# Performance work log

Measured on AMD Instinct MI355X. Metric: run time of the kernel, lower is better.

## Reference

```python
import jax, jax.numpy as jnp
import numpy as np


def _gru_dir(x, Wih, Whh, bih, bhh):
    # x: (B,T,I) -> (B,T,H); torch GRU equations, h0 = 0
    H = Whh.shape[1]
    pre = x @ Wih.T + bih  # (B,T,3H), input projection hoisted out of scan
    def step(h, p):
        gh = h @ Whh.T + bhh
        pr, pz, pn = jnp.split(p, 3, axis=-1)
        gr, gz, gn = jnp.split(gh, 3, axis=-1)
        r = jax.nn.sigmoid(pr + gr)
        z = jax.nn.sigmoid(pz + gz)
        n = jnp.tanh(pn + r * gn)
        h = (1.0 - z) * n + z * h
        return h, h
    h0 = jnp.zeros((x.shape[0], H), x.dtype)
    _, ys = jax.lax.scan(step, h0, jnp.swapaxes(pre, 0, 1))
    return jnp.swapaxes(ys, 0, 1)


def _gru_bidir(x, Wih, Whh, bih, bhh):
    f = _gru_dir(x, Wih[0], Whh[0], bih[0], bhh[0])
    b = _gru_dir(x[:, ::-1], Wih[1], Whh[1], bih[1], bhh[1])[:, ::-1]
    return jnp.concatenate([f, b], axis=-1)


def _forward(inputs, embed, l_Wih, l_Whh, l_bih, l_bhh, r_Wih, r_Whh, r_bih, r_bhh,
             a_Wih, a_Whh, a_bih, a_bhh, Wc1, Wc2, vc, Wb, Wd, vd, Wm, vm, Ws, vs,
             Wp, vp, Wpred):
    x = embed[inputs]  # (B,T,E)
    hl = _gru_bidir(x, l_Wih, l_Whh, l_bih, l_bhh)  # (B,T,2H)
    hr = _gru_bidir(x, r_Wih, r_Whh, r_bih, r_bhh)  # (B,T,2H)
    # co-attention: score[b,i,j] = vc . tanh(Wc1 hl_j + Wc2 hr_i)
    s = jnp.tanh((hl @ Wc1.T)[:, None, :, :] + (hr @ Wc2.T)[:, :, None, :])  # (B,T,T,H)
    ptc = jax.nn.softmax((s @ vc.T)[..., 0], axis=-1) @ hl
    # bilinear: hr (Wb hl)^T
    sjt = jnp.einsum('bid,bjd->bij', hr, hl @ Wb.T)
    ptb = jax.nn.softmax(sjt, axis=-1) @ hl
    # multiplicative: vd . tanh(Wd (hl_j * hr_i))
    p = hl[:, None, :, :] * hr[:, :, None, :]  # (B,T,T,2H)
    ptd = jax.nn.softmax((jnp.tanh(p @ Wd.T) @ vd.T)[..., 0], axis=-1) @ hl
    # subtractive: vm . tanh(Wm (hl_j - hr_i))
    d = hl[:, None, :, :] - hr[:, :, None, :]  # (B,T,T,2H)
    ptm = jax.nn.softmax((jnp.tanh(d @ Wm.T) @ vm.T)[..., 0], axis=-1) @ hl
    # self-attention on hr: vs . tanh(Ws (hr_j * hr_i))
    ss = hr[:, None, :, :] * hr[:, :, None, :]  # (B,T,T,2H)
    pts = jax.nn.softmax((jnp.tanh(ss @ Ws.T) @ vs.T)[..., 0], axis=-1) @ hr
    agg = jnp.concatenate([hr, pts, ptc, ptd, ptb, ptm], axis=-1)  # (B,T,12H)
    ar = _gru_bidir(agg, a_Wih, a_Whh, a_bih, a_bhh)  # (B,T,2H)
    # pooling of hl
    sj = jax.nn.softmax(jnp.swapaxes(jnp.tanh(hl @ Wp.T) @ vp.T, 1, 2), axis=-1)  # (B,1,T)
    rl = sj @ hl  # (B,1,2H)
    # final attention over aggregation
    sj2 = jax.nn.softmax(jnp.swapaxes((ar @ Wc1.T + rl @ Wc2.T) @ vc.T, 1, 2), axis=-1)  # (B,1,T)
    rr = (sj2 @ ar)[:, 0, :]  # (B,2H)
    return jax.nn.sigmoid(rr @ Wpred.T)  # (B,labels)


def setup_inputs() -> dict:
    B, T, V, E, H, L = 4, 256, 30000, 300, 128, 2
    key = jax.random.key(0)
    ks = jax.random.split(key, 40)
    inp = {}
    inp['inputs'] = jax.random.randint(ks[0], (B, T), 0, V)
    inp['embed'] = jax.random.uniform(ks[1], (V, E), jnp.float32, -0.1, 0.1)
    ki = 2
    for name, isz in [('l', E), ('r', E), ('a', 12 * H)]:
        inp[name + '_Wih'] = jax.random.normal(ks[ki], (2, 3 * H, isz), jnp.float32) * 0.05; ki += 1
        inp[name + '_Whh'] = jax.random.normal(ks[ki], (2, 3 * H, H), jnp.float32) * 0.05; ki += 1
        inp[name + '_bih'] = jnp.zeros((2, 3 * H), jnp.float32)
        inp[name + '_bhh'] = jnp.zeros((2, 3 * H), jnp.float32)
    for n, o, i in [('Wc1', H, 2 * H), ('Wc2', H, 2 * H), ('vc', 1, H), ('Wb', 2 * H, 2 * H),
                    ('Wd', H, 2 * H), ('vd', 1, H), ('Wm', H, 2 * H), ('vm', 1, H),
                    ('Ws', H, 2 * H), ('vs', 1, H), ('Wp', H, 2 * H), ('vp', 1, H),
                    ('Wpred', L, 2 * H)]:
        inp[n] = jax.random.normal(ks[ki], (o, i), jnp.float32) * 0.05; ki += 1
    return inp


def reference(inputs, embed, l_Wih, l_Whh, l_bih, l_bhh, r_Wih, r_Whh, r_bih, r_bhh,
              a_Wih, a_Whh, a_bih, a_bhh, Wc1, Wc2, vc, Wb, Wd, vd, Wm, vm, Ws, vs,
              Wp, vp, Wpred):
    return _forward(inputs, embed, l_Wih, l_Whh, l_bih, l_bhh, r_Wih, r_Whh, r_bih,
                    r_bhh, a_Wih, a_Whh, a_bih, a_bhh, Wc1, Wc2, vc, Wb, Wd, vd, Wm,
                    vm, Ws, vs, Wp, vp, Wpred)
```

## Files before the change

kernel.cpp:

```cpp
#include <hip/hip_runtime.h>


#define DEV static __device__ __forceinline__
#define BAR_LGKM() __asm__ volatile("s_waitcnt lgkmcnt(0)\ns_barrier" ::: "memory")

typedef __attribute__((ext_vector_type(4))) float f32x4;
typedef __attribute__((ext_vector_type(8))) short s16x8;
typedef __attribute__((ext_vector_type(4))) unsigned int u32x4;

constexpr int T = 256, E = 300, EP = 320, H = 128, H2 = 256, H3 = 384, H12 = 1536;
constexpr int M = 1024;
constexpr int STY = 262144;

DEV float b2f(unsigned short h) { return __uint_as_float(((unsigned)h) << 16); }
DEV unsigned short f2b(float f) {
  unsigned u = __float_as_uint(f);
  u += 0x7fff + ((u >> 16) & 1);
  return (unsigned short)(u >> 16);
}
DEV unsigned cvt_pk_bf16(float lo, float hi) {
  unsigned r;
  __asm__("v_cvt_pk_bf16_f32 %0, %1, %2" : "=v"(r) : "v"(lo), "v"(hi));
  return r;
}
DEV float rcp_f(float x) {
  float r;
  __asm__("v_rcp_f32 %0, %1" : "=v"(r) : "v"(x));
  return r;
}
DEV float sigm(float x) { return rcp_f(1.f + __expf(-x)); }
DEV float tanh_f(float x) {
  float e = __expf(2.f * x);
  return __builtin_fmaf(-2.f, rcp_f(e + 1.f), 1.f);
}

DEV s16x8 ldfrag(const unsigned short* p) {
  u32x4 v = *(const u32x4*)p;
  return __builtin_bit_cast(s16x8, v);
}
DEV f32x4 mfma16(s16x8 a, s16x8 b, f32x4 c) {
  return __builtin_amdgcn_mfma_f32_16x16x32_bf16(a, b, c, 0, 0, 0);
}


struct StageArgs {
  const float* cs[9]; unsigned short* cd[9]; int cn[9];
  const int* idx; const float* emb; unsigned short* xhi; unsigned short* xlo;
  const float* lW; const float* rW; unsigned short* wpad;
};

__global__ void k_stage(StageArgs sa) {
  int seg = blockIdx.y;
  int i = blockIdx.x * 256 + threadIdx.x;
  if (seg < 9) {
    if (i < sa.cn[seg]) sa.cd[seg][i] = f2b(sa.cs[seg][i]);
    return;
  }
  if (seg == 9) {
    if (i >= M * EP) return;
    int m = i / EP, e = i - m * EP;
    int r = sa.idx[m];
    float v = (e < E) ? sa.emb[(size_t)r * E + e] : 0.f;
    unsigned short hi = f2b(v);
    sa.xhi[i] = hi;
    sa.xlo[i] = f2b(v - b2f(hi));
    return;
  }
  if (i >= 4 * H3 * EP) return;
  int e = i % EP, n = (i / EP) % H3, uu = i / (EP * H3);
  const float* src = (uu < 2 ? sa.lW : sa.rW) + (size_t)((uu & 1) * H3 + n) * E;
  sa.wpad[i] = (e < E) ? f2b(src[e]) : (unsigned short)0;
}


struct GemmDesc {
  const unsigned short* Ahi; const unsigned short* Alo; const unsigned short* W;
  const float* bias; float* Cf; int N; int K;
};
struct GemmBatch { GemmDesc d[8]; };

__global__ __launch_bounds__(256) void k_gemm(GemmBatch gb) {
  GemmDesc g = gb.d[blockIdx.z];
  int nb = blockIdx.y * 64;
  if (nb >= g.N) return;
  int mb = blockIdx.x * 64;
  int lane = threadIdx.x & 63, w = threadIdx.x >> 6, quad = lane >> 4, l16 = lane & 15;
  int K = g.K;
  const unsigned short* Ahp = g.Ahi + (size_t)(mb + w * 16 + l16) * K + quad * 8;
  const unsigned short* Alp = g.Alo + (size_t)(mb + w * 16 + l16) * K + quad * 8;
  const unsigned short* Wp = g.W + (size_t)(nb + l16) * K + quad * 8;
  f32x4 acc[4];
  #pragma unroll
  for (int nt = 0; nt < 4; ++nt) acc[nt] = f32x4{0.f, 0.f, 0.f, 0.f};
  for (int k = 0; k < K; k += 32) {
    s16x8 ah = ldfrag(Ahp + k);
    s16x8 al = ldfrag(Alp + k);
    #pragma unroll
    for (int nt = 0; nt < 4; ++nt) {
      s16x8 b = ldfrag(Wp + (size_t)nt * 16 * K + k);
      acc[nt] = mfma16(ah, b, acc[nt]);
      acc[nt] = mfma16(al, b, acc[nt]);
    }
  }
  int mr0 = mb + w * 16 + quad * 4;
  #pragma unroll
  for (int nt = 0; nt < 4; ++nt) {
    int col = nb + nt * 16 + l16;
    float bv = g.bias ? g.bias[col] : 0.f;
    #pragma unroll
    for (int r = 0; r < 4; ++r)
      g.Cf[(size_t)(mr0 + r) * g.N + col] = acc[nt][r] + bv;
  }
}


struct RecArgs {
  const unsigned short* whh[4];
  const float* pre[4];
  float* outf[4];
  unsigned short* outhi[4];
  unsigned short* outlo[4];
  unsigned short* agghi[4];
  unsigned short* agglo[4];
  const float* bhh[4];
  int colOff[4];
  int dir[4];
};

__global__ __launch_bounds__(512) void k_gru(RecArgs ra) {
  int u = blockIdx.x;
  __shared__ __align__(16) unsigned short hs[2][16 * 136];
  int tid = threadIdx.x, lane = tid & 63, w8 = tid >> 6;
  int quad = lane >> 4, l16 = lane & 15;
  for (int i = tid; i < 2 * 16 * 136; i += 512) ((unsigned short*)hs)[i] = 0;
  const unsigned short* whh = ra.whh[u];
  s16x8 bq[3][4];
  #pragma unroll
  for (int g = 0; g < 3; ++g) {
    int row = g * 128 + w8 * 16 + l16;
    #pragma unroll
    for (int kc = 0; kc < 4; ++kc)
      bq[g][kc] = ldfrag(whh + (size_t)row * H + kc * 32 + quad * 8);
  }
  const float* bhh = ra.bhh[u];
  const float* pre = ra.pre[u];
  float* outf = ra.outf[u];
  unsigned short* outhi = ra.outhi[u];
  unsigned short* outlo = ra.outlo[u];
  unsigned short* agghi = ra.agghi[u];
  unsigned short* agglo = ra.agglo[u];
  int colOff = ra.colOff[u], dir = ra.dir[u];
  int b = ((quad & 1) << 1) | (quad >> 1);
  int d = w8 * 16 + l16;
  float bh_r = bhh[d], bh_z = bhh[d + 128], bh_n = bhh[d + 256];
  float hf = 0.f;
  float ob[8];
  unsigned short obh[8], obl[8];
  int t0 = dir ? (T - 1) : 0;
  const float* pq = pre + (size_t)(b * T + t0) * H3 + d;
  float n_pr = pq[0], n_pz = pq[128], n_pn = pq[256];
  long pst = dir ? -(long)H3 : (long)H3;
  __syncthreads();
  for (int sb = 0; sb < T; sb += 8) {
    #pragma unroll
    for (int ss = 0; ss < 8; ++ss) {
      float pr = n_pr, pz = n_pz, pn = n_pn;
      pq += pst;
      n_pr = pq[0]; n_pz = pq[128]; n_pn = pq[256];
      const unsigned short* hcur = hs[ss & 1];
      unsigned short* hnxt = hs[(ss & 1) ^ 1];
      s16x8 ah[4];
      #pragma unroll
      for (int kc = 0; kc < 4; ++kc)
        ah[kc] = ldfrag(hcur + l16 * 136 + kc * 32 + quad * 8);
      f32x4 accA[3], accB[3];
      #pragma unroll
      for (int g = 0; g < 3; ++g) {
        accA[g] = f32x4{0.f, 0.f, 0.f, 0.f};
        accB[g] = f32x4{0.f, 0.f, 0.f, 0.f};
      }
      #pragma unroll
      for (int g = 0; g < 3; ++g) accA[g] = mfma16(ah[0], bq[g][0], accA[g]);
      #pragma unroll
      for (int g = 0; g < 3; ++g) accB[g] = mfma16(ah[2], bq[g][2], accB[g]);
      #pragma unroll
      for (int g = 0; g < 3; ++g) accA[g] = mfma16(ah[1], bq[g][1], accA[g]);
      #pragma unroll
      for (int g = 0; g < 3; ++g) accB[g] = mfma16(ah[3], bq[g][3], accB[g]);
      float ghv[3];
      #pragma unroll
      for (int g = 0; g < 3; ++g) {
        float x0 = (accA[g][0] + accB[g][0]) + (accA[g][1] + accB[g][1]);
        float x1 = (accA[g][2] + accB[g][2]) + (accA[g][3] + accB[g][3]);
        float y1 = __shfl_xor(x1, 32);
        ghv[g] = (quad >= 2) ? y1 : x0;
      }
      float rg = sigm(pr + ghv[0] + bh_r);
      float zg = sigm(pz + ghv[1] + bh_z);
      float ng = tanh_f(pn + rg * (ghv[2] + bh_n));
      hf = (1.f - zg) * ng + zg * hf;
      unsigned short hi = f2b(hf);
      unsigned short lo = f2b(hf - b2f(hi));
      hnxt[(2 * b) * 136 + d] = hi;
      hnxt[(2 * b + 1) * 136 + d] = lo;
      ob[ss] = hf; obh[ss] = hi; obl[ss] = lo;
      BAR_LGKM();
    }
    #pragma unroll
    for (int qq = 0; qq < 8; ++qq) {
      int sq = sb + qq;
      int tq = dir ? (T - 1 - sq) : sq;
      size_t o = (size_t)(b * T + tq) * H2 + colOff + d;
      outf[o] = ob[qq]; outhi[o] = obh[qq]; outlo[o] = obl[qq];
      if (agghi) {
        size_t a = (size_t)(b * T + tq) * H12 + colOff + d;
        agghi[a] = obh[qq]; agglo[a] = obl[qq];
      }
    }
  }
}


struct ScArgs {
  const unsigned short* Xhi[2];
  const float* Rf; const float* Wt[2]; const float* vt[2];
  float* So[2]; float* So2[2];
  const float *Hc, *Rc, *Hm, *Rm, *HB, *hrf, *vcf, *vmf; float* S;
};

__global__ __launch_bounds__(256, 4) void k_score(ScArgs a) {
  __shared__ __align__(16) unsigned char smem[34816];
  int which = blockIdx.y;
  int bi = blockIdx.x, b = bi >> 8;
  int tid = threadIdx.x;
  if (which == 4) {
    float* rc_l = (float*)smem;
    float* rm_l = rc_l + 128;
    float* vc_l = rm_l + 128;
    float* vm_l = vc_l + 128;
    float* hr_l = vm_l + 128;
    if (tid < 128) {
      rc_l[tid] = a.Rc[(size_t)bi * 128 + tid];
      rm_l[tid] = a.Rm[(size_t)bi * 128 + tid];
      vc_l[tid] = a.vcf[tid];
      vm_l[tid] = a.vmf[tid];
    }
    hr_l[tid] = a.hrf[(size_t)bi * 256 + tid];
    __syncthreads();
    int j = tid;
    const float4* hc4 = (const float4*)(a.Hc + (size_t)(b * 256 + j) * 128);
    const float4* hm4 = (const float4*)(a.Hm + (size_t)(b * 256 + j) * 128);
    const float4* hb4 = (const float4*)(a.HB + (size_t)(b * 256 + j) * 256);
    const float4* rc4 = (const float4*)rc_l;
    const float4* rm4 = (const float4*)rm_l;
    const float4* vc4 = (const float4*)vc_l;
    const float4* vm4 = (const float4*)vm_l;
    const float4* hr4 = (const float4*)hr_l;
    float sc = 0.f, sm = 0.f, sb2 = 0.f;
    #pragma unroll 4
    for (int k = 0; k < 32; ++k) {
      float4 x = hc4[k], c = rc4[k], v = vc4[k];
      sc += v.x * tanh_f(x.x + c.x) + v.y * tanh_f(x.y + c.y)
          + v.z * tanh_f(x.z + c.z) + v.w * tanh_f(x.w + c.w);
      float4 am = hm4[k], cm = rm4[k], vv = vm4[k];
      sm += vv.x * tanh_f(am.x - cm.x) + vv.y * tanh_f(am.y - cm.y)
          + vv.z * tanh_f(am.z - cm.z) + vv.w * tanh_f(am.w - cm.w);
    }
    #pragma unroll 4
    for (int k = 0; k < 64; ++k) {
      float4 p = hb4[k], h = hr4[k];
      sb2 += p.x * h.x + p.y * h.y + p.z * h.z + p.w * h.w;
    }
    size_t o = (size_t)bi * 256 + j;
    a.S[(size_t)STY * 1 + o] = sc;
    a.S[(size_t)STY * 3 + o] = sb2;
    a.S[(size_t)STY * 4 + o] = sm;
    return;
  }
  int type = which >> 1, khb = which & 1;
  const unsigned short* Xhi = a.Xhi[type];
  const float* W = a.Wt[type] + (size_t)khb * 64 * 256;
  const float* v = a.vt[type] + khb * 64;
  float* Sout = khb ? a.So2[type] : a.So[type];
  unsigned short* w_lds = (unsigned short*)smem;
  float* sp = (float*)(smem + 32768);
  int lane = tid & 63, w = tid >> 6, quad = lane >> 4, l16 = lane & 15;
  int cp = w & 1, jh = w >> 1;
  int d4 = tid & 63, rhi = tid >> 6;
  float4 h4 = ((const float4*)(a.Rf + (size_t)bi * 256))[d4];
  #pragma unroll
  for (int it = 0; it < 16; ++it) {
    int kl = it * 4 + rhi;
    float4 w4 = ((const float4*)(W + (size_t)kl * 256))[d4];
    unsigned lo32 = cvt_pk_bf16(w4.x * h4.x, w4.y * h4.y);
    unsigned hi32 = cvt_pk_bf16(w4.z * h4.z, w4.w * h4.w);
    unsigned long long pk = (unsigned long long)lo32 | ((unsigned long long)hi32 << 32);
    int gphys = ((d4 >> 1) + kl) & 31;
    *(unsigned long long*)(w_lds + (size_t)kl * 256 + gphys * 8 + (d4 & 1) * 4) = pk;
  }
  BAR_LGKM();
  s16x8 afr[2][8];
  #pragma unroll
  for (int c = 0; c < 2; ++c) {
    int krow = cp * 32 + c * 16 + l16;
    #pragma unroll
    for (int kc = 0; kc < 8; ++kc) {
      int gp = (kc * 4 + quad + krow) & 31;
      afr[c][kc] = ldfrag(w_lds + (size_t)krow * 256 + gp * 8);
    }
  }
  float vv[2][4];
  #pragma unroll
  for (int c = 0; c < 2; ++c)
    #pragma unroll
    for (int r = 0; r < 4; ++r) vv[c][r] = v[cp * 32 + c * 16 + quad * 4 + r];
  #pragma unroll
  for (int jj = 0; jj < 8; ++jj) {
    int jt = jh * 8 + jj;
    const unsigned short* Xp = Xhi + (size_t)(b * 256 + jt * 16 + l16) * 256 + quad * 8;
    s16x8 bf[8];
    #pragma unroll
    for (int kc = 0; kc < 8; ++kc) bf[kc] = ldfrag(Xp + kc * 32);
    f32x4 acc[2];
    acc[0] = f32x4{0.f, 0.f, 0.f, 0.f};
    acc[1] = f32x4{0.f, 0.f, 0.f, 0.f};
    #pragma unroll
    for (int kc = 0; kc < 8; ++kc) {
      acc[0] = mfma16(afr[0][kc], bf[kc], acc[0]);
      acc[1] = mfma16(afr[1][kc], bf[kc], acc[1]);
    }
    float s = 0.f;
    #pragma unroll
    for (int c = 0; c < 2; ++c)
      #pragma unroll
      for (int r = 0; r < 4; ++r) s += tanh_f(acc[c][r]) * vv[c][r];
    s += __shfl_xor(s, 16);
    s += __shfl_xor(s, 32);
    if (lane < 16) sp[cp * 256 + jt * 16 + l16] = s;
  }
  BAR_LGKM();
  Sout[(size_t)bi * 256 + tid] = sp[tid] + sp[256 + tid];
}


__global__ __launch_bounds__(256) void k_wsum(const float* __restrict__ S,
    const float* __restrict__ S2,
    const float* __restrict__ hl_f, const float* __restrict__ hr_f,
    unsigned short* __restrict__ ahi, unsigned short* __restrict__ alo) {
  int it = blockIdx.x, type = blockIdx.y, b = blockIdx.z;
  __shared__ float p_l[8][256];
  __shared__ float red[4];
  int tid = threadIdx.x;
  for (int ii = 0; ii < 8; ++ii) {
    size_t idx = ((size_t)(b * 256 + it * 8 + ii)) * 256 + tid;
    float x = S[(size_t)type * STY + idx];
    if (type == 0) x += S2[idx];
    else if (type == 2) x += S2[(size_t)STY + idx];
    float m = x;
    for (int dl = 32; dl; dl >>= 1) m = fmaxf(m, __shfl_xor(m, dl));
    if ((tid & 63) == 0) red[tid >> 6] = m;
    __syncthreads();
    m = fmaxf(fmaxf(red[0], red[1]), fmaxf(red[2], red[3]));
    __syncthreads();
    float e = __expf(x - m);
    float sum = e;
    for (int dl = 32; dl; dl >>= 1) sum += __shfl_xor(sum, dl);
    if ((tid & 63) == 0) red[tid >> 6] = sum;
    __syncthreads();
    sum = red[0] + red[1] + red[2] + red[3];
    p_l[ii][tid] = e * rcp_f(sum);
    __syncthreads();
  }
  const float* src = (type == 0 ? hr_f : hl_f) + (size_t)b * 256 * 256;
  float acc[8] = {0.f, 0.f, 0.f, 0.f, 0.f, 0.f, 0.f, 0.f};
  for (int j = 0; j < 256; ++j) {
    float hv = src[(size_t)j * 256 + tid];
    #pragma unroll
    for (int ii = 0; ii < 8; ++ii) acc[ii] += p_l[ii][j] * hv;
  }
  int off = 256 * (1 + type);
  #pragma unroll
  for (int ii = 0; ii < 8; ++ii) {
    float vv = acc[ii];
    unsigned short hi = f2b(vv);
    size_t o = (size_t)(b * 256 + it * 8 + ii) * H12 + off + tid;
    ahi[o] = hi;
    alo[o] = f2b(vv - b2f(hi));
  }
}


__global__ __launch_bounds__(256) void k_tail(const float* __restrict__ Hp,
    const float* __restrict__ hl_f, const float* __restrict__ vpf,
    const float* __restrict__ Wc2f, const float* __restrict__ Arc,
    const float* __restrict__ ar_f, const float* __restrict__ vcf,
    const float* __restrict__ Wpredf, float* __restrict__ out) {
  int b = blockIdx.x, tid = threadIdx.x;
  __shared__ float vl[128], wl[256], rvec[256], rlcl[128], red[4];
  if (tid < 128) vl[tid] = vpf[tid];
  __syncthreads();
  const float* hp = Hp + (size_t)(b * 256 + tid) * 128;
  float s = 0.f;
  for (int k = 0; k < 128; ++k) s += vl[k] * tanh_f(hp[k]);
  float m = s;
  for (int dl = 32; dl; dl >>= 1) m = fmaxf(m, __shfl_xor(m, dl));
  if ((tid & 63) == 0) red[tid >> 6] = m;
  __syncthreads();
  m = fmaxf(fmaxf(red[0], red[1]), fmaxf(red[2], red[3]));
  __syncthreads();
  float e = __expf(s - m);
  float sum = e;
  for (int dl = 32; dl; dl >>= 1) sum += __shfl_xor(sum, dl);
  if ((tid & 63) == 0) red[tid >> 6] = sum;
  __syncthreads();
  sum = red[0] + red[1] + red[2] + red[3];
  wl[tid] = e * rcp_f(sum);
  __syncthreads();
  float acc = 0.f;
  for (int t = 0; t < 256; ++t) acc += wl[t] * hl_f[(size_t)(b * 256 + t) * 256 + tid];
  rvec[tid] = acc;
  __syncthreads();
  if (tid < 128) {
    float a2 = 0.f;
    const float* wr = Wc2f + (size_t)tid * 256;
    for (int dk = 0; dk < 256; ++dk) a2 += rvec[dk] * wr[dk];
    rlcl[tid] = a2;
    vl[tid] = vcf[tid];
  }
  __syncthreads();
  const float* ap = Arc + (size_t)(b * 256 + tid) * 128;
  float s2 = 0.f;
  for (int k = 0; k < 128; ++k) s2 += vl[k] * (ap[k] + rlcl[k]);
  m = s2;
  for (int dl = 32; dl; dl >>= 1) m = fmaxf(m, __shfl_xor(m, dl));
  if ((tid & 63) == 0) red[tid >> 6] = m;
  __syncthreads();
  m = fmaxf(fmaxf(red[0], red[1]), fmaxf(red[2], red[3]));
  __syncthreads();
  float e2 = __expf(s2 - m);
  float sum2 = e2;
  for (int dl = 32; dl; dl >>= 1) sum2 += __shfl_xor(sum2, dl);
  if ((tid & 63) == 0) red[tid >> 6] = sum2;
  __syncthreads();
  sum2 = red[0] + red[1] + red[2] + red[3];
  wl[tid] = e2 * rcp_f(sum2);
  __syncthreads();
  float acc2 = 0.f;
  for (int t = 0; t < 256; ++t) acc2 += wl[t] * ar_f[(size_t)(b * 256 + t) * 256 + tid];
  rvec[tid] = acc2;
  __syncthreads();
  if (tid < 2) {
    float o = 0.f;
    const float* wp = Wpredf + (size_t)tid * 256;
    for (int dk = 0; dk < 256; ++dk) o += rvec[dk] * wp[dk];
    out[b * 2 + tid] = sigm(o);
  }
}


extern "C" void kernel_launch(void* const* d_in, const int* in_sizes, int n_in,
                              void* d_out, int out_size, void* d_ws, size_t ws_size,
                              hipStream_t stream) {
  (void)in_sizes; (void)n_in; (void)out_size; (void)ws_size;
  const int* inputs = (const int*)d_in[0];
  const float* embed = (const float*)d_in[1];
  const float* lWih = (const float*)d_in[2];
  const float* lWhh = (const float*)d_in[3];
  const float* lbih = (const float*)d_in[4];
  const float* lbhh = (const float*)d_in[5];
  const float* rWih = (const float*)d_in[6];
  const float* rWhh = (const float*)d_in[7];
  const float* rbih = (const float*)d_in[8];
  const float* rbhh = (const float*)d_in[9];
  const float* aWih = (const float*)d_in[10];
  const float* aWhh = (const float*)d_in[11];
  const float* abih = (const float*)d_in[12];
  const float* abhh = (const float*)d_in[13];
  const float* Wc1 = (const float*)d_in[14];
  const float* Wc2 = (const float*)d_in[15];
  const float* vc  = (const float*)d_in[16];
  const float* Wb  = (const float*)d_in[17];
  const float* Wd  = (const float*)d_in[18];
  const float* vd  = (const float*)d_in[19];
  const float* Wm  = (const float*)d_in[20];
  const float* vmv = (const float*)d_in[21];
  const float* Wsw = (const float*)d_in[22];
  const float* vsv = (const float*)d_in[23];
  const float* Wp  = (const float*)d_in[24];
  const float* vp  = (const float*)d_in[25];
  const float* Wpred = (const float*)d_in[26];

  char* ws = (char*)d_ws;
  size_t off = 0;
  auto alloc = [&](size_t bytes) -> void* {
    void* p = ws + off;
    off += (bytes + 255) & ~(size_t)255;
    return p;
  };
  unsigned short* xhi = (unsigned short*)alloc((size_t)M * EP * 2);
  unsigned short* xlo = (unsigned short*)alloc((size_t)M * EP * 2);
  unsigned short* wpad = (unsigned short*)alloc((size_t)4 * H3 * EP * 2);
  unsigned short* Whh_b = (unsigned short*)alloc((size_t)6 * H3 * H * 2);
  unsigned short* aWih_b = (unsigned short*)alloc((size_t)2 * H3 * H12 * 2);
  unsigned short* Wc1_b = (unsigned short*)alloc((size_t)H * H2 * 2);
  unsigned short* Wc2_b = (unsigned short*)alloc((size_t)H * H2 * 2);
  unsigned short* Wm_b  = (unsigned short*)alloc((size_t)H * H2 * 2);
  unsigned short* Wp_b  = (unsigned short*)alloc((size_t)H * H2 * 2);
  unsigned short* Wb_b  = (unsigned short*)alloc((size_t)H2 * H2 * 2);
  char* region1 = (char*)alloc((size_t)4 * M * H3 * 4);
  float* pre_lr = (float*)region1;
  float* S      = (float*)region1;
  float* pre_a  = (float*)region1;
  float* S2 = (float*)alloc((size_t)2 * STY * 4);
  float* hl_f = (float*)alloc((size_t)M * H2 * 4);
  float* hr_f = (float*)alloc((size_t)M * H2 * 4);
  unsigned short* hl_hi = (unsigned short*)alloc((size_t)M * H2 * 2);
  unsigned short* hl_lo = (unsigned short*)alloc((size_t)M * H2 * 2);
  unsigned short* hr_hi = (unsigned short*)alloc((size_t)M * H2 * 2);
  unsigned short* hr_lo = (unsigned short*)alloc((size_t)M * H2 * 2);
  float* Hc = (float*)alloc((size_t)M * H * 4);
  float* Rc = (float*)alloc((size_t)M * H * 4);
  float* Hm = (float*)alloc((size_t)M * H * 4);
  float* Rm = (float*)alloc((size_t)M * H * 4);
  float* Hp = (float*)alloc((size_t)M * H * 4);
  float* HB = (float*)alloc((size_t)M * H2 * 4);
  unsigned short* agg_hi = (unsigned short*)alloc((size_t)M * H12 * 2);
  unsigned short* agg_lo = (unsigned short*)alloc((size_t)M * H12 * 2);
  float* ar_f = (float*)alloc((size_t)M * H2 * 4);
  unsigned short* ar_hi = (unsigned short*)alloc((size_t)M * H2 * 2);
  unsigned short* ar_lo = (unsigned short*)alloc((size_t)M * H2 * 2);
  float* Arc = (float*)alloc((size_t)M * H * 4);

  StageArgs sa{};
  sa.cs[0] = lWhh;  sa.cd[0] = Whh_b;                 sa.cn[0] = 2 * H3 * H;
  sa.cs[1] = rWhh;  sa.cd[1] = Whh_b + 2 * H3 * H;    sa.cn[1] = 2 * H3 * H;
  sa.cs[2] = aWhh;  sa.cd[2] = Whh_b + 4 * H3 * H;    sa.cn[2] = 2 * H3 * H;
  sa.cs[3] = aWih;  sa.cd[3] = aWih_b;                sa.cn[3] = 2 * H3 * H12;
  sa.cs[4] = Wc1;   sa.cd[4] = Wc1_b;                 sa.cn[4] = H * H2;
  sa.cs[5] = Wc2;   sa.cd[5] = Wc2_b;                 sa.cn[5] = H * H2;
  sa.cs[6] = Wm;    sa.cd[6] = Wm_b;                  sa.cn[6] = H * H2;
  sa.cs[7] = Wp;    sa.cd[7] = Wp_b;                  sa.cn[7] = H * H2;
  sa.cs[8] = Wb;    sa.cd[8] = Wb_b;                  sa.cn[8] = H2 * H2;
  sa.idx = inputs; sa.emb = embed; sa.xhi = xhi; sa.xlo = xlo;
  sa.lW = lWih; sa.rW = rWih; sa.wpad = wpad;
  k_stage<<<dim3((2 * H3 * H12 + 255) / 256, 11), dim3(256), 0, stream>>>(sa);

  GemmBatch ga{};
  const float* biases[4] = { lbih, lbih + H3, rbih, rbih + H3 };
  for (int u = 0; u < 4; ++u)
    ga.d[u] = GemmDesc{ xhi, xlo, wpad + (size_t)u * H3 * EP, biases[u],
                        pre_lr + (size_t)u * M * H3, H3, EP };
  k_gemm<<<dim3(16, 6, 4), dim3(256), 0, stream>>>(ga);

  RecArgs r1{};
  r1.whh[0] = Whh_b;               r1.whh[1] = Whh_b + H3 * H;
  r1.whh[2] = Whh_b + 2 * H3 * H;  r1.whh[3] = Whh_b + 3 * H3 * H;
  for (int u = 0; u < 4; ++u) r1.pre[u] = pre_lr + (size_t)u * M * H3;
  r1.outf[0] = r1.outf[1] = hl_f; r1.outf[2] = r1.outf[3] = hr_f;
  r1.outhi[0] = r1.outhi[1] = hl_hi; r1.outhi[2] = r1.outhi[3] = hr_hi;
  r1.outlo[0] = r1.outlo[1] = hl_lo; r1.outlo[2] = r1.outlo[3] = hr_lo;
  r1.agghi[0] = r1.agghi[1] = nullptr; r1.agghi[2] = r1.agghi[3] = agg_hi;
  r1.agglo[0] = r1.agglo[1] = nullptr; r1.agglo[2] = r1.agglo[3] = agg_lo;
  r1.bhh[0] = lbhh; r1.bhh[1] = lbhh + H3; r1.bhh[2] = rbhh; r1.bhh[3] = rbhh + H3;
  r1.colOff[0] = 0; r1.colOff[1] = H; r1.colOff[2] = 0; r1.colOff[3] = H;
  r1.dir[0] = 0; r1.dir[1] = 1; r1.dir[2] = 0; r1.dir[3] = 1;
  k_gru<<<dim3(4), dim3(512), 0, stream>>>(r1);

  GemmBatch gbB{};
  gbB.d[0] = GemmDesc{ hl_hi, hl_lo, Wc1_b, nullptr, Hc, H, H2 };
  gbB.d[1] = GemmDesc{ hr_hi, hr_lo, Wc2_b, nullptr, Rc, H, H2 };
  gbB.d[2] = GemmDesc{ hl_hi, hl_lo, Wm_b, nullptr, Hm, H, H2 };
  gbB.d[3] = GemmDesc{ hr_hi, hr_lo, Wm_b, nullptr, Rm, H, H2 };
  gbB.d[4] = GemmDesc{ hl_hi, hl_lo, Wb_b, nullptr, HB, H2, H2 };
  gbB.d[5] = GemmDesc{ hl_hi, hl_lo, Wp_b, nullptr, Hp, H, H2 };
  k_gemm<<<dim3(16, 4, 6), dim3(256), 0, stream>>>(gbB);

  ScArgs sc{};
  sc.Xhi[0] = hl_hi; sc.Wt[0] = Wd;  sc.vt[0] = vd;  sc.So[0] = S + (size_t)2 * STY;
  sc.Xhi[1] = hr_hi; sc.Wt[1] = Wsw; sc.vt[1] = vsv; sc.So[1] = S + (size_t)0 * STY;
  sc.So2[0] = S2 + (size_t)STY;
  sc.So2[1] = S2;
  sc.Rf = hr_f;
  sc.Hc = Hc; sc.Rc = Rc; sc.Hm = Hm; sc.Rm = Rm; sc.HB = HB;
  sc.hrf = hr_f; sc.vcf = vc; sc.vmf = vmv; sc.S = S;
  k_score<<<dim3(M, 5), dim3(256), 0, stream>>>(sc);

  k_wsum<<<dim3(32, 5, 4), dim3(256), 0, stream>>>(S, S2, hl_f, hr_f, agg_hi, agg_lo);

  GemmBatch gc{};
  gc.d[0] = GemmDesc{ agg_hi, agg_lo, aWih_b, abih, pre_a, H3, H12 };
  gc.d[1] = GemmDesc{ agg_hi, agg_lo, aWih_b + (size_t)H3 * H12, abih + H3,
                      pre_a + (size_t)M * H3, H3, H12 };
  k_gemm<<<dim3(16, 6, 2), dim3(256), 0, stream>>>(gc);

  RecArgs r2{};
  r2.whh[0] = Whh_b + 4 * H3 * H; r2.whh[1] = Whh_b + 5 * H3 * H;
  r2.whh[2] = r2.whh[3] = Whh_b + 4 * H3 * H;
  r2.pre[0] = pre_a; r2.pre[1] = pre_a + (size_t)M * H3;
  r2.pre[2] = r2.pre[3] = pre_a;
  r2.outf[0] = r2.outf[1] = r2.outf[2] = r2.outf[3] = ar_f;
  r2.outhi[0] = r2.outhi[1] = r2.outhi[2] = r2.outhi[3] = ar_hi;
  r2.outlo[0] = r2.outlo[1] = r2.outlo[2] = r2.outlo[3] = ar_lo;
  for (int u = 0; u < 4; ++u) { r2.agghi[u] = nullptr; r2.agglo[u] = nullptr; }
  r2.bhh[0] = abhh; r2.bhh[1] = abhh + H3; r2.bhh[2] = r2.bhh[3] = abhh;
  r2.colOff[0] = 0; r2.colOff[1] = H; r2.colOff[2] = r2.colOff[3] = 0;
  r2.dir[0] = 0; r2.dir[1] = 1; r2.dir[2] = r2.dir[3] = 0;
  k_gru<<<dim3(2), dim3(512), 0, stream>>>(r2);

  GemmBatch gd{};
  gd.d[0] = GemmDesc{ ar_hi, ar_lo, Wc1_b, nullptr, Arc, H, H2 };
  k_gemm<<<dim3(16, 2, 1), dim3(256), 0, stream>>>(gd);

  k_tail<<<dim3(4), dim3(256), 0, stream>>>(Hp, hl_f, vp, Wc2, Arc, ar_f, vc, Wpred,
                                            (float*)d_out);
}
```

Before: 754.4 us.

## Transpose Hc/Hm/HB outputs and batch eight query rows per score block

The GEMM gains a transposed-store option so Hc, Hm and HB are written column-major. The elementwise score path (which==4) then processes eight query rows per block with coalesced per-k loads, reusing each loaded column value eight times instead of re-reading it for every row. The MFMA score path now has each wave handle all 64 k-rows for 4 j-tiles and write results directly, dropping the LDS reduction and second barrier. The cost is more registers, a lower occupancy bound (launch_bounds 256,2), and uncoalesced transposed stores in the GEMM.

```diff
diff --git a/kernel.cpp b/kernel.cpp
--- a/kernel.cpp
+++ b/kernel.cpp
@@ -75,7 +75,7 @@
 
 struct GemmDesc {
   const unsigned short* Ahi; const unsigned short* Alo; const unsigned short* W;
-  const float* bias; float* Cf; int N; int K;
+  const float* bias; float* Cf; int N; int K; int tr;
 };
 struct GemmBatch { GemmDesc d[8]; };
 
@@ -108,8 +108,12 @@
     int col = nb + nt * 16 + l16;
     float bv = g.bias ? g.bias[col] : 0.f;
     #pragma unroll
-    for (int r = 0; r < 4; ++r)
-      g.Cf[(size_t)(mr0 + r) * g.N + col] = acc[nt][r] + bv;
+    for (int r = 0; r < 4; ++r) {
+      if (g.tr)
+        g.Cf[(size_t)col * M + (mr0 + r)] = acc[nt][r] + bv;
+      else
+        g.Cf[(size_t)(mr0 + r) * g.N + col] = acc[nt][r] + bv;
+    }
   }
 }
 
@@ -228,64 +232,68 @@
   const float *Hc, *Rc, *Hm, *Rm, *HB, *hrf, *vcf, *vmf; float* S;
 };
 
-__global__ __launch_bounds__(256, 4) void k_score(ScArgs a) {
-  __shared__ __align__(16) unsigned char smem[34816];
+__global__ __launch_bounds__(256, 2) void k_score(ScArgs a) {
+  __shared__ __align__(16) unsigned char smem[32768];
   int which = blockIdx.y;
-  int bi = blockIdx.x, b = bi >> 8;
+  int bi = blockIdx.x;
   int tid = threadIdx.x;
   if (which == 4) {
+    if (bi >= 128) return;
+    int b = bi >> 5, i0 = (bi & 31) << 3;
+    int gi0 = b * 256 + i0;
     float* rc_l = (float*)smem;
-    float* rm_l = rc_l + 128;
-    float* vc_l = rm_l + 128;
+    float* rm_l = rc_l + 1024;
+    float* hr_l = rm_l + 1024;
+    float* vc_l = hr_l + 2048;
     float* vm_l = vc_l + 128;
-    float* hr_l = vm_l + 128;
-    if (tid < 128) {
-      rc_l[tid] = a.Rc[(size_t)bi * 128 + tid];
-      rm_l[tid] = a.Rm[(size_t)bi * 128 + tid];
-      vc_l[tid] = a.vcf[tid];
-      vm_l[tid] = a.vmf[tid];
-    }
-    hr_l[tid] = a.hrf[(size_t)bi * 256 + tid];
+    {
+      const float4* rc4 = (const float4*)(a.Rc + (size_t)gi0 * 128);
+      const float4* rm4 = (const float4*)(a.Rm + (size_t)gi0 * 128);
+      ((float4*)rc_l)[tid] = rc4[tid];
+      ((float4*)rm_l)[tid] = rm4[tid];
+      const float4* hr4 = (const float4*)(a.hrf + (size_t)gi0 * 256);
+      ((float4*)hr_l)[tid] = hr4[tid];
+      ((float4*)hr_l)[256 + tid] = hr4[256 + tid];
+      if (tid < 128) { vc_l[tid] = a.vcf[tid]; vm_l[tid] = a.vmf[tid]; }
+    }
     __syncthreads();
     int j = tid;
-    const float4* hc4 = (const float4*)(a.Hc + (size_t)(b * 256 + j) * 128);
-    const float4* hm4 = (const float4*)(a.Hm + (size_t)(b * 256 + j) * 128);
-    const float4* hb4 = (const float4*)(a.HB + (size_t)(b * 256 + j) * 256);
-    const float4* rc4 = (const float4*)rc_l;
-    const float4* rm4 = (const float4*)rm_l;
-    const float4* vc4 = (const float4*)vc_l;
-    const float4* vm4 = (const float4*)vm_l;
-    const float4* hr4 = (const float4*)hr_l;
-    float sc = 0.f, sm = 0.f, sb2 = 0.f;
-    #pragma unroll 4
-    for (int k = 0; k < 32; ++k) {
-      float4 x = hc4[k], c = rc4[k], v = vc4[k];
-      sc += v.x * tanh_f(x.x + c.x) + v.y * tanh_f(x.y + c.y)
-          + v.z * tanh_f(x.z + c.z) + v.w * tanh_f(x.w + c.w);
-      float4 am = hm4[k], cm = rm4[k], vv = vm4[k];
-      sm += vv.x * tanh_f(am.x - cm.x) + vv.y * tanh_f(am.y - cm.y)
-          + vv.z * tanh_f(am.z - cm.z) + vv.w * tanh_f(am.w - cm.w);
-    }
-    #pragma unroll 4
-    for (int k = 0; k < 64; ++k) {
-      float4 p = hb4[k], h = hr4[k];
-      sb2 += p.x * h.x + p.y * h.y + p.z * h.z + p.w * h.w;
-    }
-    size_t o = (size_t)bi * 256 + j;
-    a.S[(size_t)STY * 1 + o] = sc;
-    a.S[(size_t)STY * 3 + o] = sb2;
-    a.S[(size_t)STY * 4 + o] = sm;
+    size_t cb = (size_t)(b * 256 + j);
+    float scq[8], smq[8], sbq[8];
+    #pragma unroll
+    for (int q = 0; q < 8; ++q) { scq[q] = 0.f; smq[q] = 0.f; sbq[q] = 0.f; }
+    for (int k = 0; k < 128; ++k) {
+      float hc = a.Hc[(size_t)k * M + cb];
+      float hm = a.Hm[(size_t)k * M + cb];
+      float vck = vc_l[k], vmk = vm_l[k];
+      #pragma unroll
+      for (int q = 0; q < 8; ++q) {
+        scq[q] += vck * tanh_f(hc + rc_l[q * 128 + k]);
+        smq[q] += vmk * tanh_f(hm - rm_l[q * 128 + k]);
+      }
+    }
+    for (int k = 0; k < 256; ++k) {
+      float hb = a.HB[(size_t)k * M + cb];
+      #pragma unroll
+      for (int q = 0; q < 8; ++q) sbq[q] += hb * hr_l[q * 256 + k];
+    }
+    #pragma unroll
+    for (int q = 0; q < 8; ++q) {
+      size_t o = (size_t)(gi0 + q) * 256 + j;
+      a.S[(size_t)STY * 1 + o] = scq[q];
+      a.S[(size_t)STY * 3 + o] = sbq[q];
+      a.S[(size_t)STY * 4 + o] = smq[q];
+    }
     return;
   }
   int type = which >> 1, khb = which & 1;
+  int b = bi >> 8;
   const unsigned short* Xhi = a.Xhi[type];
   const float* W = a.Wt[type] + (size_t)khb * 64 * 256;
   const float* v = a.vt[type] + khb * 64;
   float* Sout = khb ? a.So2[type] : a.So[type];
   unsigned short* w_lds = (unsigned short*)smem;
-  float* sp = (float*)(smem + 32768);
   int lane = tid & 63, w = tid >> 6, quad = lane >> 4, l16 = lane & 15;
-  int cp = w & 1, jh = w >> 1;
   int d4 = tid & 63, rhi = tid >> 6;
   float4 h4 = ((const float4*)(a.Rf + (size_t)bi * 256))[d4];
   #pragma unroll
@@ -299,47 +307,45 @@
     *(unsigned long long*)(w_lds + (size_t)kl * 256 + gphys * 8 + (d4 & 1) * 4) = pk;
   }
   BAR_LGKM();
-  s16x8 afr[2][8];
-  #pragma unroll
-  for (int c = 0; c < 2; ++c) {
-    int krow = cp * 32 + c * 16 + l16;
+  s16x8 afr[4][8];
+  #pragma unroll
+  for (int c = 0; c < 4; ++c) {
+    int krow = c * 16 + l16;
     #pragma unroll
     for (int kc = 0; kc < 8; ++kc) {
       int gp = (kc * 4 + quad + krow) & 31;
       afr[c][kc] = ldfrag(w_lds + (size_t)krow * 256 + gp * 8);
     }
   }
-  float vv[2][4];
-  #pragma unroll
-  for (int c = 0; c < 2; ++c)
-    #pragma unroll
-    for (int r = 0; r < 4; ++r) vv[c][r] = v[cp * 32 + c * 16 + quad * 4 + r];
-  #pragma unroll
-  for (int jj = 0; jj < 8; ++jj) {
-    int jt = jh * 8 + jj;
+  float vv[4][4];
+  #pragma unroll
+  for (int c = 0; c < 4; ++c)
+    #pragma unroll
+    for (int r = 0; r < 4; ++r) vv[c][r] = v[c * 16 + quad * 4 + r];
+  #pragma unroll
+  for (int jj = 0; jj < 4; ++jj) {
+    int jt = w * 4 + jj;
     const unsigned short* Xp = Xhi + (size_t)(b * 256 + jt * 16 + l16) * 256 + quad * 8;
     s16x8 bf[8];
     #pragma unroll
     for (int kc = 0; kc < 8; ++kc) bf[kc] = ldfrag(Xp + kc * 32);
-    f32x4 acc[2];
-    acc[0] = f32x4{0.f, 0.f, 0.f, 0.f};
-    acc[1] = f32x4{0.f, 0.f, 0.f, 0.f};
+    f32x4 acc[4];
+    #pragma unroll
+    for (int c = 0; c < 4; ++c) acc[c] = f32x4{0.f, 0.f, 0.f, 0.f};
     #pragma unroll
     for (int kc = 0; kc < 8; ++kc) {
-      acc[0] = mfma16(afr[0][kc], bf[kc], acc[0]);
-      acc[1] = mfma16(afr[1][kc], bf[kc], acc[1]);
+      #pragma unroll
+      for (int c = 0; c < 4; ++c) acc[c] = mfma16(afr[c][kc], bf[kc], acc[c]);
     }
     float s = 0.f;
     #pragma unroll
-    for (int c = 0; c < 2; ++c)
+    for (int c = 0; c < 4; ++c)
       #pragma unroll
       for (int r = 0; r < 4; ++r) s += tanh_f(acc[c][r]) * vv[c][r];
     s += __shfl_xor(s, 16);
     s += __shfl_xor(s, 32);
-    if (lane < 16) sp[cp * 256 + jt * 16 + l16] = s;
-  }
-  BAR_LGKM();
-  Sout[(size_t)bi * 256 + tid] = sp[tid] + sp[256 + tid];
+    if (lane < 16) Sout[(size_t)bi * 256 + jt * 16 + l16] = s;
+  }
 }
 
 
@@ -549,7 +555,7 @@
   const float* biases[4] = { lbih, lbih + H3, rbih, rbih + H3 };
   for (int u = 0; u < 4; ++u)
     ga.d[u] = GemmDesc{ xhi, xlo, wpad + (size_t)u * H3 * EP, biases[u],
-                        pre_lr + (size_t)u * M * H3, H3, EP };
+                        pre_lr + (size_t)u * M * H3, H3, EP, 0 };
   k_gemm<<<dim3(16, 6, 4), dim3(256), 0, stream>>>(ga);
 
   RecArgs r1{};
@@ -567,12 +573,12 @@
   k_gru<<<dim3(4), dim3(512), 0, stream>>>(r1);
 
   GemmBatch gbB{};
-  gbB.d[0] = GemmDesc{ hl_hi, hl_lo, Wc1_b, nullptr, Hc, H, H2 };
-  gbB.d[1] = GemmDesc{ hr_hi, hr_lo, Wc2_b, nullptr, Rc, H, H2 };
-  gbB.d[2] = GemmDesc{ hl_hi, hl_lo, Wm_b, nullptr, Hm, H, H2 };
-  gbB.d[3] = GemmDesc{ hr_hi, hr_lo, Wm_b, nullptr, Rm, H, H2 };
-  gbB.d[4] = GemmDesc{ hl_hi, hl_lo, Wb_b, nullptr, HB, H2, H2 };
-  gbB.d[5] = GemmDesc{ hl_hi, hl_lo, Wp_b, nullptr, Hp, H, H2 };
+  gbB.d[0] = GemmDesc{ hl_hi, hl_lo, Wc1_b, nullptr, Hc, H, H2, 1 };
+  gbB.d[1] = GemmDesc{ hr_hi, hr_lo, Wc2_b, nullptr, Rc, H, H2, 0 };
+  gbB.d[2] = GemmDesc{ hl_hi, hl_lo, Wm_b, nullptr, Hm, H, H2, 1 };
+  gbB.d[3] = GemmDesc{ hr_hi, hr_lo, Wm_b, nullptr, Rm, H, H2, 0 };
+  gbB.d[4] = GemmDesc{ hl_hi, hl_lo, Wb_b, nullptr, HB, H2, H2, 1 };
+  gbB.d[5] = GemmDesc{ hl_hi, hl_lo, Wp_b, nullptr, Hp, H, H2, 0 };
   k_gemm<<<dim3(16, 4, 6), dim3(256), 0, stream>>>(gbB);
 
   ScArgs sc{};
@@ -588,9 +594,9 @@
   k_wsum<<<dim3(32, 5, 4), dim3(256), 0, stream>>>(S, S2, hl_f, hr_f, agg_hi, agg_lo);
 
   GemmBatch gc{};
-  gc.d[0] = GemmDesc{ agg_hi, agg_lo, aWih_b, abih, pre_a, H3, H12 };
+  gc.d[0] = GemmDesc{ agg_hi, agg_lo, aWih_b, abih, pre_a, H3, H12, 0 };
   gc.d[1] = GemmDesc{ agg_hi, agg_lo, aWih_b + (size_t)H3 * H12, abih + H3,
-                      pre_a + (size_t)M * H3, H3, H12 };
+                      pre_a + (size_t)M * H3, H3, H12, 0 };
   k_gemm<<<dim3(16, 6, 2), dim3(256), 0, stream>>>(gc);
 
   RecArgs r2{};
@@ -608,7 +614,7 @@
   k_gru<<<dim3(2), dim3(512), 0, stream>>>(r2);
 
   GemmBatch gd{};
-  gd.d[0] = GemmDesc{ ar_hi, ar_lo, Wc1_b, nullptr, Arc, H, H2 };
+  gd.d[0] = GemmDesc{ ar_hi, ar_lo, Wc1_b, nullptr, Arc, H, H2, 0 };
   k_gemm<<<dim3(16, 2, 1), dim3(256), 0, stream>>>(gd);
 
   k_tail<<<dim3(4), dim3(256), 0, stream>>>(Hp, hl_f, vp, Wc2, Arc, ar_f, vc, Wpred,
```

Result: no change. 741.8 us (-1.7%).
